# Kernel optimization log

Measured on AMD Instinct MI355X. Metric: run time of the kernel, lower is better.

Reference implementation:

```python
import jax, jax.numpy as jnp
import numpy as np

RC = 5.0
P = 6
N_ATOM = 4
N_AXIS = 8
EPS = 1e-5
C_RES = 0.89442719  # sqrt(0.8)
C_NEW = 0.4472      # ~sqrt(0.2)
BESSEL_PREF = float(np.sqrt(2.0 / RC))


def poly_cutoff(x):
    # nequip-style PolynomialCutoff, p=6
    xr = x / RC
    p = float(P)
    out = (1.0
           - (p + 1.0) * (p + 2.0) / 2.0 * xr ** P
           + p * (p + 2.0) * xr ** (P + 1)
           - p * (p + 1.0) / 2.0 * xr ** (P + 2))
    return jnp.where(xr < 1.0, out, 0.0)


def bessel(x, w):
    # x: [E], w: [n_basis] (trainable n*pi weights)
    return BESSEL_PREF * jnp.sin(w * x[:, None] / RC) / x[:, None]


def layer_norm(x, g, b):
    m = jnp.mean(x, axis=-1, keepdims=True)
    v = jnp.var(x, axis=-1, keepdims=True)
    return (x - m) * jax.lax.rsqrt(v + EPS) * g + b


def mlp3(x, W1, b1, W2, b2, W3, b3):
    # FFN: hidden block (linear-tanh-linear) + tanh + final linear
    h = jnp.tanh(x @ W1 + b1)
    h = jnp.tanh(h @ W2 + b2)
    return h @ W3 + b3


def resnet3(x, W1, b1, W2, b2, W3, b3):
    # ResNet: residual added where in/out dims match (final 64->64 linear)
    h = jnp.tanh(x @ W1 + b1)
    h = h @ W2 + b2
    return jnp.tanh(h) @ W3 + b3 + h


def seg_mean(x, idx, n):
    s = jax.ops.segment_sum(x, idx, num_segments=n)
    c = jax.ops.segment_sum(jnp.ones((x.shape[0],), x.dtype), idx, num_segments=n)
    c = jnp.maximum(c, 1.0).reshape((n,) + (1,) * (x.ndim - 1))
    return s / c


def setup_inputs() -> dict:
    key = jax.random.key(0)
    ks = iter(jax.random.split(key, 64))
    N, E, E2 = 40000, 320000, 160000
    NB, NR, NS, NA = 16, 64, 16, 8
    D = NA * NS  # 128 = n_hidden
    L = 2
    f32 = jnp.float32

    def nrm(shape, s=0.05):
        return jax.random.normal(next(ks), shape, dtype=f32) * s

    inp = {}
    inp['atom_types'] = jax.random.randint(next(ks), (N,), 0, N_ATOM, dtype=jnp.int32)
    ev = jax.random.normal(next(ks), (E, 3), dtype=f32)
    inp['env_vectors'] = ev
    inp['env_length'] = jnp.linalg.norm(ev, axis=-1) + 0.1
    inp['edge_length'] = jax.random.uniform(next(ks), (E2,), dtype=f32) * 4.0 + 0.5
    inp['env_index'] = jax.random.randint(next(ks), (2, E), 0, N, dtype=jnp.int32)
    inp['edge_index'] = jax.random.randint(next(ks), (2, E2), 0, N, dtype=jnp.int32)
    inp['bessel_w'] = jnp.arange(1, NB + 1, dtype=f32) * jnp.pi
    A = 2 * N_ATOM + NB  # 24
    inp['sr_W1'], inp['sr_b1'] = nrm((A, 64)), nrm((64,))
    inp['sr_W2'], inp['sr_b2'] = nrm((64, 64)), nrm((64,))
    inp['sr_W3'], inp['sr_b3'] = nrm((64, NS)), nrm((NS,))
    inp['rd_W1'], inp['rd_b1'] = nrm((A, 64)), nrm((64,))
    inp['rd_W2'], inp['rd_b2'] = nrm((64, 64)), nrm((64,))
    inp['rd_W3'], inp['rd_b3'] = nrm((64, NR)), nrm((NR,))
    inp['ne_emb_W'], inp['ne_emb_b'] = nrm((NR, D)), nrm((D,))
    inp['ne_nln_g'], inp['ne_nln_b'] = jnp.ones((D,), f32), jnp.zeros((D,), f32)
    inp['ne_eln_g'], inp['ne_eln_b'] = jnp.ones((NR,), f32), jnp.zeros((NR,), f32)
    inp['ly_emb_W'], inp['ly_emb_b'] = nrm((L, NR, D)), nrm((L, D))
    inp['ly_hid_W1'], inp['ly_hid_b1'] = nrm((L, 2 * D, 128)), nrm((L, 128))
    inp['ly_hid_W2'], inp['ly_hid_b2'] = nrm((L, 128, 128)), nrm((L, 128))
    inp['ly_hid_W3'], inp['ly_hid_b3'] = nrm((L, 128, D)), nrm((L, D))
    inp['ly_rdl_W1'], inp['ly_rdl_b1'] = nrm((L, NR + D, 64)), nrm((L, 64))
    inp['ly_rdl_W2'], inp['ly_rdl_b2'] = nrm((L, 64, 64)), nrm((L, 64))
    inp['ly_rdl_W3'], inp['ly_rdl_b3'] = nrm((L, 64, NR)), nrm((L, NR))
    inp['ly_nln_g'], inp['ly_nln_b'] = jnp.ones((L, D), f32), jnp.zeros((L, D), f32)
    inp['ly_eln_g'], inp['ly_eln_b'] = jnp.ones((L, NR), f32), jnp.zeros((L, NR), f32)
    return inp


def reference(atom_types, env_vectors, env_length, edge_length, env_index, edge_index,
              bessel_w,
              sr_W1, sr_b1, sr_W2, sr_b2, sr_W3, sr_b3,
              rd_W1, rd_b1, rd_W2, rd_b2, rd_W3, rd_b3,
              ne_emb_W, ne_emb_b, ne_nln_g, ne_nln_b, ne_eln_g, ne_eln_b,
              ly_emb_W, ly_emb_b,
              ly_hid_W1, ly_hid_b1, ly_hid_W2, ly_hid_b2, ly_hid_W3, ly_hid_b3,
              ly_rdl_W1, ly_rdl_b1, ly_rdl_W2, ly_rdl_b2, ly_rdl_W3, ly_rdl_b3,
              ly_nln_g, ly_nln_b, ly_eln_g, ly_eln_b):
    N = atom_types.shape[0]
    oh = jax.nn.one_hot(atom_types, N_ATOM, dtype=env_vectors.dtype)
    # atom_attr[index].transpose(1,0).reshape(E,-1) == concat of the two endpoints' one-hots
    env_attr = jnp.concatenate([oh[env_index[0]], oh[env_index[1]]], -1)   # [E, 2*n_atom]
    edge_attr = jnp.concatenate([oh[edge_index[0]], oh[edge_index[1]]], -1)
    ud_env = poly_cutoff(env_length)[:, None]    # [E, 1]
    ud_edge = poly_cutoff(edge_length)[:, None]  # [E2, 1]
    feat_env = jnp.concatenate([env_attr, ud_env * bessel(env_length, bessel_w)], -1)
    feat_edge = jnp.concatenate([edge_attr, ud_edge * bessel(edge_length, bessel_w)], -1)
    env_sqrt = mlp3(feat_env, sr_W1, sr_b1, sr_W2, sr_b2, sr_W3, sr_b3) * ud_env  # [E, n_sqrt]
    env_radial = layer_norm(mlp3(feat_env, rd_W1, rd_b1, rd_W2, rd_b2, rd_W3, rd_b3), ne_eln_g, ne_eln_b) * ud_env
    edge_radial = layer_norm(mlp3(feat_edge, rd_W1, rd_b1, rd_W2, rd_b2, rd_W3, rd_b3), ne_eln_g, ne_eln_b) * ud_edge
    # SE(2) aggregation: msg = [env_sqrt | ud * env_vectors]; outer product per node
    msg = env_sqrt[:, :, None] * (ud_env * env_vectors)[:, None, :]  # [E, n_sqrt, 3]
    agg = seg_mean(msg, env_index[1], N)                             # [N, n_sqrt, 3]
    gram = jnp.einsum('nds,nes->nde', agg, agg)[:, :, :N_AXIS]       # [N, n_sqrt, n_axis]
    node_emb = layer_norm(gram.reshape(N, -1), ne_nln_g, ne_nln_b)   # [N, D]
    env_hidden = (env_radial @ ne_emb_W + ne_emb_b) * (node_emb[env_index[1]] + node_emb[env_index[0]]) * 0.5
    edge_hidden = (edge_radial @ ne_emb_W + ne_emb_b) * (node_emb[edge_index[1]] + node_emb[edge_index[0]]) * 0.5
    for l in range(ly_emb_W.shape[0]):
        env_weight = env_radial @ ly_emb_W[l] + ly_emb_b[l]  # [E, D]
        agg2 = seg_mean(env_weight * node_emb[env_index[1]], env_index[1], N)
        node_emb = C_RES * node_emb + C_NEW * layer_norm(agg2, ly_nln_g[l], ly_nln_b[l])
        env_hidden = mlp3(jnp.concatenate([node_emb[env_index[0]], env_hidden], -1),
                          ly_hid_W1[l], ly_hid_b1[l], ly_hid_W2[l], ly_hid_b2[l], ly_hid_W3[l], ly_hid_b3[l])
        edge_hidden = mlp3(jnp.concatenate([node_emb[edge_index[0]], edge_hidden], -1),
                           ly_hid_W1[l], ly_hid_b1[l], ly_hid_W2[l], ly_hid_b2[l], ly_hid_W3[l], ly_hid_b3[l])
        env_radial = C_RES * env_radial + C_NEW * ud_env * layer_norm(
            resnet3(jnp.concatenate([env_radial, env_hidden], -1),
                    ly_rdl_W1[l], ly_rdl_b1[l], ly_rdl_W2[l], ly_rdl_b2[l], ly_rdl_W3[l], ly_rdl_b3[l]),
            ly_eln_g[l], ly_eln_b[l])
        edge_radial = C_RES * edge_radial + C_NEW * ud_edge * layer_norm(
            resnet3(jnp.concatenate([edge_radial, edge_hidden], -1),
                    ly_rdl_W1[l], ly_rdl_b1[l], ly_rdl_W2[l], ly_rdl_b2[l], ly_rdl_W3[l], ly_rdl_b3[l]),
            ly_eln_g[l], ly_eln_b[l])
    return env_radial, edge_radial, node_emb, env_hidden, edge_hidden
```

## Files before the change

kernel.cpp:

```cpp
#include <hip/hip_runtime.h>
#include <math.h>

#define C_RES 0.89442719f
#define C_NEW 0.4472f
#define LN_EPS 1e-5f
#define BESSEL_PREF 0.6324555320336759f
#define RC_INV 0.2f

typedef __attribute__((ext_vector_type(8))) short short8;
typedef __attribute__((ext_vector_type(8))) unsigned short u16x8;
typedef __attribute__((ext_vector_type(16))) float f32x16;

__device__ __forceinline__ float fast_tanh(float x) {
  float ax = fabsf(x);
  float e = __expf(2.0f * ax);
  float t = 1.0f - 2.0f / (e + 1.0f);
  return copysignf(t, x);
}

__device__ __forceinline__ unsigned short f2b(float f) {
  unsigned int u = __float_as_uint(f);
  unsigned int r = (u + 0x7FFFu + ((u >> 16) & 1u)) >> 16;
  return (unsigned short)r;
}

__device__ __forceinline__ u16x8 cvt8(const float* s) {
  const float4 v0 = *(const float4*)s;
  const float4 v1 = *(const float4*)(s + 4);
  u16x8 w;
  w[0]=f2b(v0.x); w[1]=f2b(v0.y); w[2]=f2b(v0.z); w[3]=f2b(v0.w);
  w[4]=f2b(v1.x); w[5]=f2b(v1.y); w[6]=f2b(v1.z); w[7]=f2b(v1.w);
  return w;
}

__device__ __forceinline__ short8 cvt8s(const float* s) {
  const float4 v0 = *(const float4*)s;
  const float4 v1 = *(const float4*)(s + 4);
  short8 w;
  w[0]=(short)f2b(v0.x); w[1]=(short)f2b(v0.y); w[2]=(short)f2b(v0.z); w[3]=(short)f2b(v0.w);
  w[4]=(short)f2b(v1.x); w[5]=(short)f2b(v1.y); w[6]=(short)f2b(v1.z); w[7]=(short)f2b(v1.w);
  return w;
}

__device__ __forceinline__ float poly_cutoff(float x) {
  float xr = x * RC_INV;
  if (xr >= 1.0f) return 0.0f;
  float x2 = xr * xr;
  float x3 = x2 * xr;
  float x6 = x3 * x3;
  return 1.0f - 28.0f * x6 + 48.0f * x6 * xr - 21.0f * x6 * x2;
}

__device__ __forceinline__ int swz(int s, int kc) {
  return s ^ ((s >> 5) << 1) ^ ((kc & 1) << 2);
}

// ... 28 lines not shown
      if (lane >= o) incl += t;
    }
    if (lane == 63) wsum[wid] = incl;
    __syncthreads();
    if (wid == 0) {
      const int wv = (lane < 16) ? wsum[lane] : 0;
      int wsc = wv;
      #pragma unroll
      for (int o = 1; o < 16; o <<= 1) {
        const int t = __shfl_up(wsc, o);
        if (lane >= o) wsc += t;
      }
      if (lane < 16) wsum[lane] = wsc - wv;
    }
    __syncthreads();
    const int c0 = carry;
    const int excl = c0 + wsum[wid] + incl - v;
    if (i < n) { eoff[i] = excl; ecur[i] = excl; }
    __syncthreads();
    if (tid == 1023) carry = c0 + wsum[15] + incl;
    __syncthreads();
  }
  if (tid == 0) eoff[n] = carry;
}

__global__ void scatter_kernel(int E, const int* __restrict__ idx,
                               int* __restrict__ ecur, int* __restrict__ perm) {
  int t = blockIdx.x * 256 + threadIdx.x;
  if (t < E) {
    const int pos = atomicAdd(&ecur[idx[E + t]], 1);
    perm[pos] = t;
  }
}

__global__ void pack_hid_weights(const float* __restrict__ W1,
                                 const float* __restrict__ W2,
                                 const float* __restrict__ W3,
                                 unsigned short* __restrict__ out)
{
  int t = blockIdx.x * 256 + threadIdx.x;
  if (t >= 131072) return;
  int l = t >> 16;
  int oidx = t & 65535;
  const float* src;
  int midx;
  if (oidx < 32768)      { src = W1 + l * 32768; midx = oidx; }
  else if (oidx < 49152) { src = W2 + l * 16384; midx = oidx - 32768; }
  else                   { src = W3 + l * 16384; midx = oidx - 49152; }
  int j = midx & 7;
  int lane = (midx >> 3) & 63;
  int blk = midx >> 9;
  int ct = blk & 3, kc = blk >> 2;
  int col = ct * 32 + (lane & 31);
  int k = kc * 16 + (lane >> 5) * 8 + j;
  out[l * 65536 + oidx] = f2b(src[k * 128 + col]);
}

__global__ void pack_rdl_weights(const float* __restrict__ W1,
                                 const float* __restrict__ W2,
                                 const float* __restrict__ W3,
                                 unsigned short* __restrict__ out)
{
  int t = blockIdx.x * 256 + threadIdx.x;
  if (t >= 40960) return;
  int l = t / 20480;
  int o = t - l * 20480;
// ... 37 lines not shown
}

__global__ void pack_emb_weights(const float* __restrict__ W,
                                 unsigned short* __restrict__ out)
{
  int t = blockIdx.x * 256 + threadIdx.x;
  if (t >= 8192) return;
  const int j = t & 7, lane = (t >> 3) & 63, blk = t >> 9;
  const int ct = blk & 3, kc = blk >> 2;
  const int col = ct * 32 + (lane & 31);
  const int k = kc * 16 + (lane >> 5) * 8 + j;
  out[t] = f2b(W[k * 128 + col]);
}


#define FEAT_TRANS(BASEBLK, V0, V1) do {                                        \
    _Pragma("unroll")                                                           \
    for (int ct_ = 0; ct_ < 2; ++ct_) {                                         \
      const int colh_ = ct_*32 + cl;                                            \
      const int kc2_  = colh_ >> 4;                                             \
      const int b3_   = (colh_ >> 3) & 1;                                       \
      const int jj_   = colh_ & 7;                                              \
      const int blk_  = ((BASEBLK) + kc2_*3 + wave)*512;                        \
      _Pragma("unroll")                                                         \
      for (int q_ = 0; q_ < 16; ++q_) {                                         \
        const int row32_ = (q_ & 3) + 8*(q_ >> 2) + 4*(lane >> 5);              \
        const int s2_ = (row32_ & 31) + 32*b3_;                                 \
        const float v_ = ct_ ? (V1)[q_] : (V0)[q_];                             \
        afrag[blk_ + swz(s2_, kc2_)*8 + jj_] = f2b(fast_tanh(v_));              \
      }                                                                         \
    }                                                                           \
  } while (0)

template<int HAS_SR>
__launch_bounds__(192)
__global__ void feat_mfma(
    int nrows,
    const int* __restrict__ types, const float* __restrict__ lens,
    const float* __restrict__ vecs, const int* __restrict__ idx,
    const float* __restrict__ bessel_w,
    const unsigned short* __restrict__ wpackf,
    const float* __restrict__ srb1, const float* __restrict__ srb2,
    const float* __restrict__ srb3,
    const float* __restrict__ rdb1, const float* __restrict__ rdb2,
    const float* __restrict__ rdb3,
    const float* __restrict__ eln_g, const float* __restrict__ eln_b,
    float* __restrict__ radial_out, float* __restrict__ ud_out,
    float* __restrict__ msgbuf)
{
  __shared__ __align__(16) unsigned short afrag[30*512];
  __shared__ __align__(16) unsigned short wlds[36*512];
  __shared__ float udl[96];

  const int tid  = threadIdx.x;
  const int lane = tid & 63;
  const int wave = tid >> 6;
  const int base = blockIdx.x * 96;
  const int cl   = lane & 31;

  for (int i = tid; i < 2304; i += 192)
    *(u16x8*)&wlds[i*8] = *(const u16x8*)&wpackf[i*8];

  {
    const int r = tid >> 1, h = tid & 1;
    int rowc = base + r;
    const bool valid = rowc < nrows;
    if (!valid) rowc = nrows - 1;
    const int i0 = idx[rowc];
    const int i1 = idx[nrows + rowc];
    const float len = lens[rowc];
    const float ud = poly_cutoff(len);
    const int t0 = types[i0], t1 = types[i1];
    const float invl = 1.0f / len;
    const int rt = r >> 5;
    #pragma unroll
    for (int m = 0; m < 12; ++m) {
      const int k = h + m*2;
      float v;
      if (k < 4)      v = (t0 == k) ? 1.0f : 0.0f;
      else if (k < 8) v = (t1 == (k-4)) ? 1.0f : 0.0f;
      else            v = ud * BESSEL_PREF * __sinf(bessel_w[k-8] * len * RC_INV) * invl;
      const int kc = k >> 4;
      const int s_ = (r & 31) + 32*((k >> 3) & 1);
      afrag[(kc*3 + rt)*512 + swz(s_, kc)*8 + (k & 7)] = f2b(v);
    }
    #pragma unroll
    for (int m = 0; m < 4; ++m) {
      const int k = 24 + h + m*2;
      const int s_ = (r & 31) + 32*((k >> 3) & 1);
      afrag[(1*3 + rt)*512 + swz(s_, 1)*8 + (k & 7)] = 0;
    }
    if (h == 0) {
      udl[r] = ud;
      if (valid) {
        ud_out[rowc] = ud;
        if (HAS_SR) {
          msgbuf[(size_t)rowc*20 + 16] = ud * vecs[(size_t)rowc*3 + 0];
          msgbuf[(size_t)rowc*20 + 17] = ud * vecs[(size_t)rowc*3 + 1];
          msgbuf[(size_t)rowc*20 + 18] = ud * vecs[(size_t)rowc*3 + 2];
        }
      }
    }
  }
  __syncthreads();

  f32x16 acc0, acc1;

  {
    const float bv0 = rdb1[cl], bv1 = rdb1[32 + cl];
    #pragma unroll
    for (int q = 0; q < 16; ++q) { acc0[q] = bv0; acc1[q] = bv1; }
  }
  #pragma unroll
  for (int kc = 0; kc < 2; ++kc) {
    const short8 a  = *(const short8*)&afrag[(kc*3 + wave)*512 + swz(lane, kc)*8];
    const short8 w0 = *(const short8*)&wlds[(kc*2 + 0)*512 + lane*8];
    const short8 w1 = *(const short8*)&wlds[(kc*2 + 1)*512 + lane*8];
    acc0 = __builtin_amdgcn_mfma_f32_32x32x16_bf16(a, w0, acc0, 0, 0, 0);
    acc1 = __builtin_amdgcn_mfma_f32_32x32x16_bf16(a, w1, acc1, 0, 0, 0);
  }
  FEAT_TRANS(6, acc0, acc1);

  {
    const float bv0 = rdb2[cl], bv1 = rdb2[32 + cl];
    #pragma unroll
    for (int q = 0; q < 16; ++q) { acc0[q] = bv0; acc1[q] = bv1; }
  }
  #pragma unroll
  for (int kc = 0; kc < 4; ++kc) {
// ... 13 lines not shown
  #pragma unroll
  for (int kc = 0; kc < 4; ++kc) {
    const short8 a  = *(const short8*)&afrag[((18 + kc*3) + wave)*512 + swz(lane, kc)*8];
    const short8 w0 = *(const short8*)&wlds[(12 + kc*2 + 0)*512 + lane*8];
    const short8 w1 = *(const short8*)&wlds[(12 + kc*2 + 1)*512 + lane*8];
    acc0 = __builtin_amdgcn_mfma_f32_32x32x16_bf16(a, w0, acc0, 0, 0, 0);
    acc1 = __builtin_amdgcn_mfma_f32_32x32x16_bf16(a, w1, acc1, 0, 0, 0);
  }
  {
    const float eg0 = eln_g[cl],      eb0 = eln_b[cl];
    const float eg1 = eln_g[32 + cl], eb1 = eln_b[32 + cl];
    #pragma unroll
    for (int q = 0; q < 16; ++q) {
      const float v0 = acc0[q], v1 = acc1[q];
      float s = v0 + v1, ss = v0*v0 + v1*v1;
      #pragma unroll
      for (int o = 1; o <= 16; o <<= 1) {
        s  += __shfl_xor(s, o);
        ss += __shfl_xor(ss, o);
      }
      const float m   = s * (1.0f/64.0f);
      const float inv = rsqrtf(ss * (1.0f/64.0f) - m*m + LN_EPS);
      const int row32 = (q & 3) + 8*(q >> 2) + 4*(lane >> 5);
      const int rloc  = wave*32 + row32;
      const int row   = base + rloc;
      if (row < nrows) {
        const float u = udl[rloc];
        radial_out[(size_t)row*64 + cl]      = ((v0 - m)*inv*eg0 + eb0) * u;
        radial_out[(size_t)row*64 + 32 + cl] = ((v1 - m)*inv*eg1 + eb1) * u;
      }
    }
  }

  if (HAS_SR) {
    {
      const float bv0 = srb1[cl], bv1 = srb1[32 + cl];
      #pragma unroll
      for (int q = 0; q < 16; ++q) { acc0[q] = bv0; acc1[q] = bv1; }
    }
    #pragma unroll
    for (int kc = 0; kc < 2; ++kc) {
      const short8 a  = *(const short8*)&afrag[(kc*3 + wave)*512 + swz(lane, kc)*8];
      const short8 w0 = *(const short8*)&wlds[(20 + kc*2 + 0)*512 + lane*8];
      const short8 w1 = *(const short8*)&wlds[(20 + kc*2 + 1)*512 + lane*8];
      acc0 = __builtin_amdgcn_mfma_f32_32x32x16_bf16(a, w0, acc0, 0, 0, 0);
      acc1 = __builtin_amdgcn_mfma_f32_32x32x16_bf16(a, w1, acc1, 0, 0, 0);
    }
    FEAT_TRANS(6, acc0, acc1);

    {
      const float bv0 = srb2[cl], bv1 = srb2[32 + cl];
      #pragma unroll
      for (int q = 0; q < 16; ++q) { acc0[q] = bv0; acc1[q] = bv1; }
    }
    #pragma unroll
    for (int kc = 0; kc < 4; ++kc) {
      const short8 a  = *(const short8*)&afrag[((6 + kc*3) + wave)*512 + swz(lane, kc)*8];
      const short8 w0 = *(const short8*)&wlds[(24 + kc*2 + 0)*512 + lane*8];
      const short8 w1 = *(const short8*)&wlds[(24 + kc*2 + 1)*512 + lane*8];
      acc0 = __builtin_amdgcn_mfma_f32_32x32x16_bf16(a, w0, acc0, 0, 0, 0);
      acc1 = __builtin_amdgcn_mfma_f32_32x32x16_bf16(a, w1, acc1, 0, 0, 0);
    }
    FEAT_TRANS(18, acc0, acc1);

    {
      const float bv0 = (cl < 16) ? srb3[cl] : 0.0f;
      #pragma unroll
// ... 134 lines not shown
  const float g0 = g[j0], g1 = g[j0+1], g2 = g[j0+2], g3 = g[j0+3];
  const float bb0 = b[j0], bb1 = b[j0+1], bb2 = b[j0+2], bb3 = b[j0+3];
  #pragma unroll
  for (int i = 0; i < 4; ++i) {
    const int n = base + r0 + i;
    if (n >= N) continue;
    const float mask = (ecnt[n] > 0) ? 1.0f : 0.0f;
    const float4 old = *(const float4*)&node_emb[(size_t)n*128 + j0];
    const float x0 = old.x * acc[i][0] * mask;
    const float x1 = old.y * acc[i][1] * mask;
    const float x2 = old.z * acc[i][2] * mask;
    const float x3 = old.w * acc[i][3] * mask;
    float s = x0 + x1 + x2 + x3;
    float ss = x0*x0 + x1*x1 + x2*x2 + x3*x3;
    #pragma unroll
    for (int o = 1; o <= 16; o <<= 1) {
      s  += __shfl_xor(s, o);
      ss += __shfl_xor(ss, o);
    }
    const float m = s * (1.0f/128.0f);
    const float inv = rsqrtf(ss * (1.0f/128.0f) - m*m + LN_EPS);
    float4 o4;
    o4.x = C_RES*old.x + C_NEW*((x0 - m)*inv*g0 + bb0);
    o4.y = C_RES*old.y + C_NEW*((x1 - m)*inv*g1 + bb1);
    o4.z = C_RES*old.z + C_NEW*((x2 - m)*inv*g2 + bb2);
    o4.w = C_RES*old.w + C_NEW*((x3 - m)*inv*g3 + bb3);
    *(float4*)&node_emb[(size_t)n*128 + j0] = o4;
  }
}


__launch_bounds__(192)
__global__ void emb_mfma(
    int nrows,
    const float* __restrict__ radial,
    const unsigned short* __restrict__ wpck, const float* __restrict__ bias,
    const int* __restrict__ idx,
    const float* __restrict__ node_emb,
    float* __restrict__ out)
{
  __shared__ __align__(16) unsigned short afrag[12*512];
  __shared__ __align__(16) unsigned short wlds[16*512];
  __shared__ int i0l[96], i1l[96];

  const int tid = threadIdx.x, lane = tid & 63, wave = tid >> 6;
  const int base = blockIdx.x * 96, cl = lane & 31;

  for (int i = tid; i < 1024; i += 192)
    *(u16x8*)&wlds[i*8] = *(const u16x8*)&wpck[i*8];

  {
    const int r = tid >> 1, h = tid & 1;
    int rowg = base + r;
    if (rowg >= nrows) rowg = nrows - 1;
    if (h == 0) { i0l[r] = idx[rowg]; i1l[r] = idx[nrows + rowg]; }
    const float* rsrc = radial + (size_t)rowg * 64;
    #pragma unroll
    for (int g = 0; g < 4; ++g) {
      const int k = h*32 + g*8;
      const u16x8 w = cvt8(rsrc + k);
      const int kc = k >> 4;
      const int s_ = (r & 31) + 32*((k >> 3) & 1);
      *(u16x8*)&afrag[(kc*3 + (r>>5))*512 + swz(s_, kc)*8] = w;
    }
  }
  __syncthreads();

  f32x16 acc0, acc1, acc2, acc3;
  {
    const float bv0 = bias[cl], bv1 = bias[32+cl];
    const float bv2 = bias[64+cl], bv3 = bias[96+cl];
    #pragma unroll
    for (int q = 0; q < 16; ++q) { acc0[q]=bv0; acc1[q]=bv1; acc2[q]=bv2; acc3[q]=bv3; }
  }
  #pragma unroll
  for (int kc = 0; kc < 4; ++kc) {
    const short8 a  = *(const short8*)&afrag[(kc*3 + wave)*512 + swz(lane, kc)*8];
    const short8 w0 = *(const short8*)&wlds[(kc*4 + 0)*512 + lane*8];
    const short8 w1 = *(const short8*)&wlds[(kc*4 + 1)*512 + lane*8];
// ... 2 lines not shown
    acc0 = __builtin_amdgcn_mfma_f32_32x32x16_bf16(a, w0, acc0, 0, 0, 0);
    acc1 = __builtin_amdgcn_mfma_f32_32x32x16_bf16(a, w1, acc1, 0, 0, 0);
    acc2 = __builtin_amdgcn_mfma_f32_32x32x16_bf16(a, w2, acc2, 0, 0, 0);
    acc3 = __builtin_amdgcn_mfma_f32_32x32x16_bf16(a, w3, acc3, 0, 0, 0);
  }

  #pragma unroll
  for (int q = 0; q < 16; ++q) {
    const int row32 = (q & 3) + 8*(q >> 2) + 4*(lane >> 5);
    const int rloc  = wave*32 + row32;
    const int row   = base + rloc;
    if (row >= nrows) continue;
    const float* n0 = node_emb + (size_t)i0l[rloc]*128;
    const float* n1 = node_emb + (size_t)i1l[rloc]*128;
    float* op = out + (size_t)row*128;
    op[cl]    = acc0[q] * 0.5f * (n0[cl]    + n1[cl]);
    op[32+cl] = acc1[q] * 0.5f * (n0[32+cl] + n1[32+cl]);
    op[64+cl] = acc2[q] * 0.5f * (n0[64+cl] + n1[64+cl]);
    op[96+cl] = acc3[q] * 0.5f * (n0[96+cl] + n1[96+cl]);
  }
}


#define STAGE_WG(SRC, OFFU16, B) do {                                           \
    _Pragma("unroll")                                                           \
    for (int i_ = 0; i_ < 2; ++i_) {                                            \
      const int c_ = tid + i_*256;                                              \
      *(u16x8*)&wg[B][c_*8] = *(const u16x8*)&(SRC)[(OFFU16) + c_*8];           \
    }                                                                           \
  } while (0)

__launch_bounds__(256, 3)
__global__ void hidrdl_mfma(
    int nrows, const int* __restrict__ idx0,
    const float* __restrict__ node_emb,
    const float* __restrict__ ud,
    const unsigned short* __restrict__ wpackh,
    const float* __restrict__ hb1, const float* __restrict__ hb2,
    const float* __restrict__ hb3,
    const unsigned short* __restrict__ wpackr,
    const float* __restrict__ rb1, const float* __restrict__ rb2,
    const float* __restrict__ rb3,
    const float* __restrict__ eln_g, const float* __restrict__ eln_b,
    float* __restrict__ hidden,
    float* __restrict__ radial)
{
  __shared__ __align__(16) unsigned short afragH[16384];
  __shared__ __align__(16) unsigned short wg[2][4096];

  const int tid  = threadIdx.x;
  const int lane = tid & 63;
  const int wave = tid >> 6;
  const int base = blockIdx.x * 128;
  const int cl   = lane & 31;
  const int khalf = lane >> 5;

  int lrow = base + wave*32 + cl;
  if (lrow >= nrows) lrow = nrows - 1;
  const int i0 = idx0[lrow];
  const float* nsrc = node_emb + (size_t)i0 * 128;
  const float* hsrc = hidden + (size_t)lrow * 128;
  const float* rsrc = radial + (size_t)lrow * 64;

  short8 aN[8], aH[8];
  #pragma unroll
  for (int kc = 0; kc < 8; ++kc) aN[kc] = cvt8s(nsrc + kc*16 + khalf*8);
  #pragma unroll
  for (int kc = 0; kc < 8; ++kc) aH[kc] = cvt8s(hsrc + kc*16 + khalf*8);

  f32x16 acc[4];

  #pragma unroll
  for (int ct = 0; ct < 4; ++ct) {
    const float bv = hb1[ct*32 + cl];
    #pragma unroll
    for (int q = 0; q < 16; ++q) acc[ct][q] = bv;
  }
  STAGE_WG(wpackh, 0, 0);
  __syncthreads();
  #pragma unroll
  for (int p = 0; p < 8; ++p) {
    if (p < 7) STAGE_WG(wpackh, (p+1)*4096, (p+1)&1);
    else       STAGE_WG(wpackh, 32768, 0);
    #pragma unroll
    for (int kcl = 0; kcl < 2; ++kcl) {
      const int kc = p*2 + kcl;
      const short8 a = (kc < 8) ? aN[kc] : aH[kc-8];
      #pragma unroll
      for (int ct = 0; ct < 4; ++ct) {
        const short8 b = *(const short8*)&wg[p&1][ (kcl*4 + ct)*512 + lane*8 ];
        acc[ct] = __builtin_amdgcn_mfma_f32_32x32x16_bf16(a, b, acc[ct], 0, 0, 0);
      }
    }
    __syncthreads();
  }

  #pragma unroll
  for (int ct = 0; ct < 4; ++ct) {
    const int kc  = ct*2 + ((lane >> 4) & 1);
    const int oct = (lane >> 3) & 1;
    const int j   = lane & 7;
    const int xk  = (oct << 1) ^ ((kc & 1) << 2);
    const int hi  = 4*(lane >> 5);
    const int bi  = (wave*8 + kc)*512 + oct*256 + j;
    #pragma unroll
    for (int q = 0; q < 16; ++q) {
      const int m32 = (q & 3) + 8*(q >> 2) + hi;
      afragH[bi + (m32 ^ xk)*8] = f2b(fast_tanh(acc[ct][q]));
    }
  }

  #pragma unroll
  for (int ct = 0; ct < 4; ++ct) {
    const float bv = hb2[ct*32 + cl];
    #pragma unroll
    for (int q = 0; q < 16; ++q) acc[ct][q] = bv;
  }
  #pragma unroll
  for (int p = 0; p < 4; ++p) {
    if (p < 3) STAGE_WG(wpackh, 32768 + (p+1)*4096, (p+1)&1);
    else       STAGE_WG(wpackh, 49152, 0);
    #pragma unroll
    for (int kcl = 0; kcl < 2; ++kcl) {
      const int kc = p*2 + kcl;
      const short8 a = *(const short8*)&afragH[ (wave*8 + kc)*512 + swz(lane, kc)*8 ];
      #pragma unroll
      for (int ct = 0; ct < 4; ++ct) {
        const short8 b = *(const short8*)&wg[p&1][ (kcl*4 + ct)*512 + lane*8 ];
        acc[ct] = __builtin_amdgcn_mfma_f32_32x32x16_bf16(a, b, acc[ct], 0, 0, 0);
      }
    }
    __syncthreads();
  }

  #pragma unroll
  for (int ct = 0; ct < 4; ++ct) {
    const int kc  = ct*2 + ((lane >> 4) & 1);
    const int oct = (lane >> 3) & 1;
    const int j   = lane & 7;
    const int xk  = (oct << 1) ^ ((kc & 1) << 2);
    const int hi  = 4*(lane >> 5);
    const int bi  = (wave*8 + kc)*512 + oct*256 + j;
    #pragma unroll
    for (int q = 0; q < 16; ++q) {
      const int m32 = (q & 3) + 8*(q >> 2) + hi;
      afragH[bi + (m32 ^ xk)*8] = f2b(fast_tanh(acc[ct][q]));
    }
  }

  #pragma unroll
  for (int ct = 0; ct < 4; ++ct) {
    const float bv = hb3[ct*32 + cl];
    #pragma unroll
    for (int q = 0; q < 16; ++q) acc[ct][q] = bv;
  }
  #pragma unroll
  for (int p = 0; p < 4; ++p) {
    if (p < 3) STAGE_WG(wpackh, 49152 + (p+1)*4096, (p+1)&1);
    else       STAGE_WG(wpackr, 0, 0);
    #pragma unroll
    for (int kcl = 0; kcl < 2; ++kcl) {
      const int kc = p*2 + kcl;
      const short8 a = *(const short8*)&afragH[ (wave*8 + kc)*512 + swz(lane, kc)*8 ];
      #pragma unroll
      for (int ct = 0; ct < 4; ++ct) {
        const short8 b = *(const short8*)&wg[p&1][ (kcl*4 + ct)*512 + lane*8 ];
        acc[ct] = __builtin_amdgcn_mfma_f32_32x32x16_bf16(a, b, acc[ct], 0, 0, 0);
      }
    }
    __syncthreads();
  }

  #pragma unroll
  for (int ct = 0; ct < 4; ++ct) {
    const int col = ct*32 + cl;
    #pragma unroll
    for (int q = 0; q < 16; ++q) {
      const int row = base + wave*32 + (q & 3) + 8*(q >> 2) + 4*khalf;
      if (row < nrows) hidden[(size_t)row*128 + col] = acc[ct][q];
    }
  }
  #pragma unroll
  for (int ct = 0; ct < 4; ++ct) {
    const int kc  = ct*2 + ((lane >> 4) & 1);
    const int oct = (lane >> 3) & 1;
    const int j   = lane & 7;
    const int xk  = (oct << 1) ^ ((kc & 1) << 2);
    const int hi  = 4*(lane >> 5);
    const int bi  = (wave*8 + kc)*512 + oct*256 + j;
    #pragma unroll
    for (int q = 0; q < 16; ++q) {
      const int m32 = (q & 3) + 8*(q >> 2) + hi;
      afragH[bi + (m32 ^ xk)*8] = f2b(acc[ct][q]);
    }
  }

  short8 aR[4];
  #pragma unroll
  for (int kc = 0; kc < 4; ++kc) aR[kc] = cvt8s(rsrc + kc*16 + khalf*8);

  f32x16 racc0, racc1;
  {
    const float bv0 = rb1[cl], bv1 = rb1[32 + cl];
    #pragma unroll
    for (int q = 0; q < 16; ++q) { racc0[q] = bv0; racc1[q] = bv1; }
  }
  #pragma unroll
  for (int t = 0; t < 3; ++t) {
    if (t < 2) STAGE_WG(wpackr, (t+1)*4096, (t+1)&1);
    else       STAGE_WG(wpackr, 12288, 1);
    #pragma unroll
    for (int kk = 0; kk < 4; ++kk) {
      const int kc = t*4 + kk;
      const short8 a = (kc < 4) ? aR[kc]
        : *(const short8*)&afragH[ (wave*8 + (kc-4))*512 + swz(lane, kc-4)*8 ];
      const short8 w0 = *(const short8*)&wg[t&1][ (kk*2 + 0)*512 + lane*8 ];
      const short8 w1 = *(const short8*)&wg[t&1][ (kk*2 + 1)*512 + lane*8 ];
      racc0 = __builtin_amdgcn_mfma_f32_32x32x16_bf16(a, w0, racc0, 0, 0, 0);
      racc1 = __builtin_amdgcn_mfma_f32_32x32x16_bf16(a, w1, racc1, 0, 0, 0);
    }
    __syncthreads();
  }

  #pragma unroll
  for (int ct = 0; ct < 2; ++ct) {
    const int colh = ct*32 + cl;
    const int kc2  = colh >> 4;
    const int b3_  = (colh >> 3) & 1;
    const int jj   = colh & 7;
    const int blk  = (wave*8 + kc2)*512;
    #pragma unroll
    for (int q = 0; q < 16; ++q) {
      const int row32 = (q & 3) + 8*(q >> 2) + 4*khalf;
      const int s_ = (row32 & 31) + 32*b3_;
      const float v = ct ? racc1[q] : racc0[q];
      afragH[blk + swz(s_, kc2)*8 + jj] = f2b(fast_tanh(v));
    }
  }

  f32x16 rh0, rh1;
  {
    const float bv0 = rb2[cl], bv1 = rb2[32 + cl];
    #pragma unroll
    for (int q = 0; q < 16; ++q) { rh0[q] = bv0; rh1[q] = bv1; }
  }
  STAGE_WG(wpackr, 16384, 0);
  #pragma unroll
  for (int kc = 0; kc < 4; ++kc) {
    const short8 a  = *(const short8*)&afragH[ (wave*8 + kc)*512 + swz(lane, kc)*8 ];
    const short8 w0 = *(const short8*)&wg[1][ (kc*2 + 0)*512 + lane*8 ];
    const short8 w1 = *(const short8*)&wg[1][ (kc*2 + 1)*512 + lane*8 ];
    rh0 = __builtin_amdgcn_mfma_f32_32x32x16_bf16(a, w0, rh0, 0, 0, 0);
    rh1 = __builtin_amdgcn_mfma_f32_32x32x16_bf16(a, w1, rh1, 0, 0, 0);
  }
  __syncthreads();

  #pragma unroll
  for (int ct = 0; ct < 2; ++ct) {
    const int colh = ct*32 + cl;
    const int kc2  = colh >> 4;
    const int b3_  = (colh >> 3) & 1;
    const int jj   = colh & 7;
    const int blk  = (wave*8 + 4 + kc2)*512;
    #pragma unroll
    for (int q = 0; q < 16; ++q) {
      const int row32 = (q & 3) + 8*(q >> 2) + 4*khalf;
      const int s_ = (row32 & 31) + 32*b3_;
      const float v = ct ? rh1[q] : rh0[q];
      afragH[blk + swz(s_, kc2)*8 + jj] = f2b(fast_tanh(v));
    }
  }

  {
    const float bv0 = rb3[cl], bv1 = rb3[32 + cl];
    #pragma unroll
    for (int q = 0; q < 16; ++q) { racc0[q] = bv0; racc1[q] = bv1; }
  }
  #pragma unroll
  for (int kc = 0; kc < 4; ++kc) {
    const short8 a  = *(const short8*)&afragH[ (wave*8 + 4 + kc)*512 + swz(lane, kc)*8 ];
    const short8 w0 = *(const short8*)&wg[0][ (kc*2 + 0)*512 + lane*8 ];
    const short8 w1 = *(const short8*)&wg[0][ (kc*2 + 1)*512 + lane*8 ];
    racc0 = __builtin_amdgcn_mfma_f32_32x32x16_bf16(a, w0, racc0, 0, 0, 0);
    racc1 = __builtin_amdgcn_mfma_f32_32x32x16_bf16(a, w1, racc1, 0, 0, 0);
  }

  const float eg0 = eln_g[cl],      eb0 = eln_b[cl];
  const float eg1 = eln_g[32 + cl], eb1 = eln_b[32 + cl];
  const float* rtile = radial + (size_t)(base + wave*32) * 64;

  #pragma unroll
  for (int q = 0; q < 16; ++q) {
    const float v0 = racc0[q] + rh0[q];
    const float v1 = racc1[q] + rh1[q];
    float s = v0 + v1, ss = v0*v0 + v1*v1;
    #pragma unroll
    for (int o = 1; o <= 16; o <<= 1) {
      s  += __shfl_xor(s, o);
      ss += __shfl_xor(ss, o);
    }
    const float m   = s * (1.0f/64.0f);
    const float inv = rsqrtf(ss * (1.0f/64.0f) - m*m + LN_EPS);
    const int row32 = (q & 3) + 8*(q >> 2) + 4*khalf;
    const int row   = base + wave*32 + row32;
    if (row < nrows) {
      const float u = ud[row];
      const float oldA = rtile[row32*64 + cl];
      const float oldB = rtile[row32*64 + 32 + cl];
      radial[(size_t)row*64 + cl]      = C_RES*oldA + C_NEW*u*((v0 - m)*inv*eg0 + eb0);
      radial[(size_t)row*64 + 32 + cl] = C_RES*oldB + C_NEW*u*((v1 - m)*inv*eg1 + eb1);
    }
  }
}


extern "C" void kernel_launch(void* const* d_in, const int* in_sizes, int n_in,
                              void* d_out, int out_size, void* d_ws, size_t ws_size,
                              hipStream_t stream)
{
  const int*   atom_types = (const int*)  d_in[0];
  const float* env_vec    = (const float*)d_in[1];
  const float* env_len    = (const float*)d_in[2];
  const float* edge_len   = (const float*)d_in[3];
  const int*   env_idx    = (const int*)  d_in[4];
  const int*   edge_idx   = (const int*)  d_in[5];
  const float* bessel_w   = (const float*)d_in[6];
  const float* srW1 = (const float*)d_in[7];  const float* srb1 = (const float*)d_in[8];
  const float* srW2 = (const float*)d_in[9];  const float* srb2 = (const float*)d_in[10];
  const float* srW3 = (const float*)d_in[11]; const float* srb3 = (const float*)d_in[12];
  const float* rdW1 = (const float*)d_in[13]; const float* rdb1 = (const float*)d_in[14];
  const float* rdW2 = (const float*)d_in[15]; const float* rdb2 = (const float*)d_in[16];
  const float* rdW3 = (const float*)d_in[17]; const float* rdb3 = (const float*)d_in[18];
  const float* ne_emb_W = (const float*)d_in[19]; const float* ne_emb_b = (const float*)d_in[20];
  const float* ne_nln_g = (const float*)d_in[21]; const float* ne_nln_b = (const float*)d_in[22];
  const float* ne_eln_g = (const float*)d_in[23]; const float* ne_eln_b = (const float*)d_in[24];
  const float* ly_emb_W = (const float*)d_in[25]; const float* ly_emb_b = (const float*)d_in[26];
  const float* ly_hid_W1 = (const float*)d_in[27]; const float* ly_hid_b1 = (const float*)d_in[28];
  const float* ly_hid_W2 = (const float*)d_in[29]; const float* ly_hid_b2 = (const float*)d_in[30];
  const float* ly_hid_W3 = (const float*)d_in[31]; const float* ly_hid_b3 = (const float*)d_in[32];
  const float* ly_rdl_W1 = (const float*)d_in[33]; const float* ly_rdl_b1 = (const float*)d_in[34];
  const float* ly_rdl_W2 = (const float*)d_in[35]; const float* ly_rdl_b2 = (const float*)d_in[36];
  const float* ly_rdl_W3 = (const float*)d_in[37]; const float* ly_rdl_b3 = (const float*)d_in[38];
  const float* ly_nln_g = (const float*)d_in[39]; const float* ly_nln_b = (const float*)d_in[40];
// ... 12 lines not shown

  float* ws = (float*)d_ws;
  float* ud_env  = ws;  ws += E;
  float* ud_edge = ws;  ws += E2;
  float* aggS    = ws;  ws += (size_t)N * 48;
  float* msgbuf  = ws;  ws += (size_t)E * 20;
  float* mean_r  = msgbuf;
  unsigned short* wpack  = (unsigned short*)ws; ws += 65536;
  unsigned short* wpack2 = (unsigned short*)ws; ws += 20480;
  unsigned short* wpack3 = (unsigned short*)ws; ws += 9216;
  unsigned short* wpackE = (unsigned short*)ws; ws += 4096;
  int* ecnt = (int*)ws; ws += N;
  int* eoff = (int*)ws; ws += N + 1;
  int* ecur = (int*)ws; ws += N + 1;
  int* perm = (int*)ws; ws += E;

  const int gEr  = (E  + 95) / 96;
  const int gE2r = (E2 + 95) / 96;
  const int gEf  = (E  + 127) / 128;
  const int gE2f = (E2 + 127) / 128;
  const int gN32 = (N + 31) / 32;
  const int gN4w = (N * 64 + 255) / 256;

  zero_int_kernel<<<256, 256, 0, stream>>>(ecnt, N);
  hist_kernel<<<(E + 255) / 256, 256, 0, stream>>>(E, env_idx, ecnt);
  scan_kernel<<<1, 1024, 0, stream>>>(ecnt, eoff, ecur, N);
  scatter_kernel<<<(E + 255) / 256, 256, 0, stream>>>(E, env_idx, ecur, perm);

  pack_hid_weights<<<512, 256, 0, stream>>>(ly_hid_W1, ly_hid_W2, ly_hid_W3, wpack);
  pack_rdl_weights<<<160, 256, 0, stream>>>(ly_rdl_W1, ly_rdl_W2, ly_rdl_W3, wpack2);
  pack_feat_weights<<<72, 256, 0, stream>>>(rdW1, rdW2, rdW3, srW1, srW2, srW3, wpack3);
  pack_emb_weights<<<32, 256, 0, stream>>>(ne_emb_W, wpackE);

  feat_mfma<1><<<gEr, 192, 0, stream>>>(E, atom_types, env_len, env_vec, env_idx, bessel_w,
      wpack3, srb1, srb2, srb3, rdb1, rdb2, rdb3,
      ne_eln_g, ne_eln_b, env_radial, ud_env, msgbuf);
  feat_mfma<0><<<gE2r, 192, 0, stream>>>(E2, atom_types, edge_len, nullptr, edge_idx, bessel_w,
      wpack3, srb1, srb2, srb3, rdb1, rdb2, rdb3,
      ne_eln_g, ne_eln_b, edge_radial, ud_edge, nullptr);

  msg_gather_kernel<<<gN4w, 256, 0, stream>>>(N, eoff, perm, msgbuf, aggS);
  node_emb_kernel<<<N, 128, 0, stream>>>(N, aggS, ecnt, ne_nln_g, ne_nln_b, node_emb);

  emb_mfma<<<gEr, 192, 0, stream>>>(E, env_radial, wpackE, ne_emb_b, env_idx, node_emb, env_hidden);
  emb_mfma<<<gE2r, 192, 0, stream>>>(E2, edge_radial, wpackE, ne_emb_b, edge_idx, node_emb, edge_hidden);

  for (int l = 0; l < 2; ++l) {
    agg_gather_kernel<<<gN4w, 256, 0, stream>>>(N, eoff, perm, env_radial, mean_r);
    node_update_gemm<<<gN32, 256, 0, stream>>>(N, mean_r, ecnt,
        ly_emb_W + (size_t)l*64*128, ly_emb_b + (size_t)l*128,
        ly_nln_g + (size_t)l*128, ly_nln_b + (size_t)l*128, node_emb);

    hidrdl_mfma<<<gEf, 256, 0, stream>>>(E, env_idx, node_emb, ud_env,
        wpack + (size_t)l*65536,
        ly_hid_b1 + (size_t)l*128, ly_hid_b2 + (size_t)l*128, ly_hid_b3 + (size_t)l*128,
        wpack2 + (size_t)l*20480,
        ly_rdl_b1 + (size_t)l*64, ly_rdl_b2 + (size_t)l*64, ly_rdl_b3 + (size_t)l*64,
        ly_eln_g + (size_t)l*64, ly_eln_b + (size_t)l*64,
        env_hidden, env_radial);
    hidrdl_mfma<<<gE2f, 256, 0, stream>>>(E2, edge_idx, node_emb, ud_edge,
        wpack + (size_t)l*65536,
        ly_hid_b1 + (size_t)l*128, ly_hid_b2 + (size_t)l*128, ly_hid_b3 + (size_t)l*128,
        wpack2 + (size_t)l*20480,
        ly_rdl_b1 + (size_t)l*64, ly_rdl_b2 + (size_t)l*64, ly_rdl_b3 + (size_t)l*64,
        ly_eln_g + (size_t)l*64, ly_eln_b + (size_t)l*64,
        edge_hidden, edge_radial);
  }
}
```

Before: 1.312 ms.

## Merge env/edge launches and stage hidrdl outputs through LDS for coalesced stores

Fuses the paired env and edge launches of feat_mfma, emb_mfma and hidrdl_mfma into single grids. Each block selects its pointer set by block index, which removes launch gaps and tail underutilisation. In hidrdl_mfma, the hidden and radial outputs are staged in LDS as bf16 and then written with row-contiguous float4 stores instead of strided scalar stores. This truncates the stored fp32 outputs to bf16 precision, which may cause accuracy drift.

```diff
diff --git a/kernel.cpp b/kernel.cpp
--- a/kernel.cpp
+++ b/kernel.cpp
@@ -22,6 +22,10 @@
   unsigned int u = __float_as_uint(f);
   unsigned int r = (u + 0x7FFFu + ((u >> 16) & 1u)) >> 16;
   return (unsigned short)r;
+}
+
+__device__ __forceinline__ float b2f(unsigned short v) {
+  return __uint_as_float((unsigned)v << 16);
 }
 
 __device__ __forceinline__ u16x8 cvt8(const float* s) {
@@ -116,6 +120,7 @@
     perm[pos] = t;
   }
 }
+
 
 __global__ void pack_hid_weights(const float* __restrict__ W1,
                                  const float* __restrict__ W2,
@@ -219,12 +224,13 @@
     }                                                                           \
   } while (0)
 
-template<int HAS_SR>
 __launch_bounds__(192)
 __global__ void feat_mfma(
-    int nrows,
-    const int* __restrict__ types, const float* __restrict__ lens,
-    const float* __restrict__ vecs, const int* __restrict__ idx,
+    int g1, int n1, const float* __restrict__ lens1, const int* __restrict__ idx1,
+    float* __restrict__ radial1, float* __restrict__ ud1,
+    int n2, const float* __restrict__ lens2, const int* __restrict__ idx2,
+    float* __restrict__ radial2, float* __restrict__ ud2,
+    const int* __restrict__ types, const float* __restrict__ vecs,
     const float* __restrict__ bessel_w,
     const unsigned short* __restrict__ wpackf,
     const float* __restrict__ srb1, const float* __restrict__ srb2,
@@ -232,7 +238,6 @@
     const float* __restrict__ rdb1, const float* __restrict__ rdb2,
     const float* __restrict__ rdb3,
     const float* __restrict__ eln_g, const float* __restrict__ eln_b,
-    float* __restrict__ radial_out, float* __restrict__ ud_out,
     float* __restrict__ msgbuf)
 {
   __shared__ __align__(16) unsigned short afrag[30*512];
@@ -242,8 +247,14 @@
   const int tid  = threadIdx.x;
   const int lane = tid & 63;
   const int wave = tid >> 6;
-  const int base = blockIdx.x * 96;
   const int cl   = lane & 31;
+
+  int blk = blockIdx.x;
+  const bool has_sr = (blk < g1);
+  int nrows; const float* lens; const int* idx; float* radial_out; float* ud_out;
+  if (has_sr) { nrows = n1; lens = lens1; idx = idx1; radial_out = radial1; ud_out = ud1; }
+  else { blk -= g1; nrows = n2; lens = lens2; idx = idx2; radial_out = radial2; ud_out = ud2; }
+  const int base = blk * 96;
 
   for (int i = tid; i < 2304; i += 192)
     *(u16x8*)&wlds[i*8] = *(const u16x8*)&wpackf[i*8];
@@ -281,7 +292,7 @@
       udl[r] = ud;
       if (valid) {
         ud_out[rowc] = ud;
-        if (HAS_SR) {
+        if (has_sr) {
           msgbuf[(size_t)rowc*20 + 16] = ud * vecs[(size_t)rowc*3 + 0];
           msgbuf[(size_t)rowc*20 + 17] = ud * vecs[(size_t)rowc*3 + 1];
           msgbuf[(size_t)rowc*20 + 18] = ud * vecs[(size_t)rowc*3 + 2];
@@ -361,7 +372,7 @@
     }
   }
 
-  if (HAS_SR) {
+  if (has_sr) {
     {
       const float bv0 = srb1[cl], bv1 = srb1[32 + cl];
       #pragma unroll
@@ -562,19 +573,25 @@
 
 __launch_bounds__(192)
 __global__ void emb_mfma(
-    int nrows,
-    const float* __restrict__ radial,
+    int g1, int n1, const float* __restrict__ radial1, const int* __restrict__ idx1,
+    float* __restrict__ out1,
+    int n2, const float* __restrict__ radial2, const int* __restrict__ idx2,
+    float* __restrict__ out2,
     const unsigned short* __restrict__ wpck, const float* __restrict__ bias,
-    const int* __restrict__ idx,
-    const float* __restrict__ node_emb,
-    float* __restrict__ out)
+    const float* __restrict__ node_emb)
 {
   __shared__ __align__(16) unsigned short afrag[12*512];
   __shared__ __align__(16) unsigned short wlds[16*512];
   __shared__ int i0l[96], i1l[96];
 
   const int tid = threadIdx.x, lane = tid & 63, wave = tid >> 6;
-  const int base = blockIdx.x * 96, cl = lane & 31;
+  const int cl = lane & 31;
+
+  int blk = blockIdx.x;
+  int nrows; const float* radial; const int* idx; float* out;
+  if (blk < g1) { nrows = n1; radial = radial1; idx = idx1; out = out1; }
+  else { blk -= g1; nrows = n2; radial = radial2; idx = idx2; out = out2; }
+  const int base = blk * 96;
 
   for (int i = tid; i < 1024; i += 192)
     *(u16x8*)&wlds[i*8] = *(const u16x8*)&wpck[i*8];
@@ -643,18 +660,19 @@
 
 __launch_bounds__(256, 3)
 __global__ void hidrdl_mfma(
-    int nrows, const int* __restrict__ idx0,
+    int g1,
+    int n1, const int* __restrict__ idx1, const float* __restrict__ ud1,
+    float* __restrict__ hid1, float* __restrict__ rad1,
+    int n2, const int* __restrict__ idx2, const float* __restrict__ ud2,
+    float* __restrict__ hid2, float* __restrict__ rad2,
     const float* __restrict__ node_emb,
-    const float* __restrict__ ud,
     const unsigned short* __restrict__ wpackh,
     const float* __restrict__ hb1, const float* __restrict__ hb2,
     const float* __restrict__ hb3,
     const unsigned short* __restrict__ wpackr,
     const float* __restrict__ rb1, const float* __restrict__ rb2,
     const float* __restrict__ rb3,
-    const float* __restrict__ eln_g, const float* __restrict__ eln_b,
-    float* __restrict__ hidden,
-    float* __restrict__ radial)
+    const float* __restrict__ eln_g, const float* __restrict__ eln_b)
 {
   __shared__ __align__(16) unsigned short afragH[16384];
   __shared__ __align__(16) unsigned short wg[2][4096];
@@ -662,9 +680,14 @@
   const int tid  = threadIdx.x;
   const int lane = tid & 63;
   const int wave = tid >> 6;
-  const int base = blockIdx.x * 128;
   const int cl   = lane & 31;
   const int khalf = lane >> 5;
+
+  int blk = blockIdx.x;
+  int nrows; const int* idx0; const float* ud; float* hidden; float* radial;
+  if (blk < g1) { nrows = n1; idx0 = idx1; ud = ud1; hidden = hid1; radial = rad1; }
+  else { blk -= g1; nrows = n2; idx0 = idx2; ud = ud2; hidden = hid2; radial = rad2; }
+  const int base = blk * 128;
 
   int lrow = base + wave*32 + cl;
   if (lrow >= nrows) lrow = nrows - 1;
@@ -712,7 +735,7 @@
     const int oct = (lane >> 3) & 1;
     const int j   = lane & 7;
     const int xk  = (oct << 1) ^ ((kc & 1) << 2);
-    const int hi  = 4*(lane >> 5);
+    const int hi  = 4*khalf;
     const int bi  = (wave*8 + kc)*512 + oct*256 + j;
     #pragma unroll
     for (int q = 0; q < 16; ++q) {
@@ -750,7 +773,7 @@
     const int oct = (lane >> 3) & 1;
     const int j   = lane & 7;
     const int xk  = (oct << 1) ^ ((kc & 1) << 2);
-    const int hi  = 4*(lane >> 5);
+    const int hi  = 4*khalf;
     const int bi  = (wave*8 + kc)*512 + oct*256 + j;
     #pragma unroll
     for (int q = 0; q < 16; ++q) {
@@ -784,25 +807,39 @@
 
   #pragma unroll
   for (int ct = 0; ct < 4; ++ct) {
-    const int col = ct*32 + cl;
-    #pragma unroll
-    for (int q = 0; q < 16; ++q) {
-      const int row = base + wave*32 + (q & 3) + 8*(q >> 2) + 4*khalf;
-      if (row < nrows) hidden[(size_t)row*128 + col] = acc[ct][q];
-    }
-  }
-  #pragma unroll
-  for (int ct = 0; ct < 4; ++ct) {
     const int kc  = ct*2 + ((lane >> 4) & 1);
     const int oct = (lane >> 3) & 1;
     const int j   = lane & 7;
     const int xk  = (oct << 1) ^ ((kc & 1) << 2);
-    const int hi  = 4*(lane >> 5);
+    const int hi  = 4*khalf;
     const int bi  = (wave*8 + kc)*512 + oct*256 + j;
     #pragma unroll
     for (int q = 0; q < 16; ++q) {
       const int m32 = (q & 3) + 8*(q >> 2) + hi;
       afragH[bi + (m32 ^ xk)*8] = f2b(acc[ct][q]);
+    }
+  }
+  {
+    const int rloc = tid >> 1;
+    const int hh = tid & 1;
+    const int row = base + rloc;
+    if (row < nrows) {
+      float* hp = hidden + (size_t)row*128 + hh*64;
+      #pragma unroll
+      for (int g = 0; g < 4; ++g) {
+        const int kc = hh*4 + g;
+        const u16x8 lo = *(const u16x8*)&afragH[(wave*8 + kc)*512 + swz((rloc & 31),      kc)*8];
+        const u16x8 hi2 = *(const u16x8*)&afragH[(wave*8 + kc)*512 + swz((rloc & 31) + 32, kc)*8];
+        float4 f0, f1, f2, f3;
+        f0.x = b2f(lo[0]); f0.y = b2f(lo[1]); f0.z = b2f(lo[2]); f0.w = b2f(lo[3]);
+        f1.x = b2f(lo[4]); f1.y = b2f(lo[5]); f1.z = b2f(lo[6]); f1.w = b2f(lo[7]);
+        f2.x = b2f(hi2[0]); f2.y = b2f(hi2[1]); f2.z = b2f(hi2[2]); f2.w = b2f(hi2[3]);
+        f3.x = b2f(hi2[4]); f3.y = b2f(hi2[5]); f3.z = b2f(hi2[6]); f3.w = b2f(hi2[7]);
+        *(float4*)(hp + g*16 + 0)  = f0;
+        *(float4*)(hp + g*16 + 4)  = f1;
+        *(float4*)(hp + g*16 + 8)  = f2;
+        *(float4*)(hp + g*16 + 12) = f3;
+      }
     }
   }
 
@@ -839,13 +876,13 @@
     const int kc2  = colh >> 4;
     const int b3_  = (colh >> 3) & 1;
     const int jj   = colh & 7;
-    const int blk  = (wave*8 + kc2)*512;
+    const int blk2 = (wave*8 + kc2)*512;
     #pragma unroll
     for (int q = 0; q < 16; ++q) {
       const int row32 = (q & 3) + 8*(q >> 2) + 4*khalf;
       const int s_ = (row32 & 31) + 32*b3_;
       const float v = ct ? racc1[q] : racc0[q];
-      afragH[blk + swz(s_, kc2)*8 + jj] = f2b(fast_tanh(v));
+      afragH[blk2 + swz(s_, kc2)*8 + jj] = f2b(fast_tanh(v));
     }
   }
 
@@ -872,13 +909,13 @@
     const int kc2  = colh >> 4;
     const int b3_  = (colh >> 3) & 1;
     const int jj   = colh & 7;
-    const int blk  = (wave*8 + 4 + kc2)*512;
+    const int blk2 = (wave*8 + 4 + kc2)*512;
     #pragma unroll
     for (int q = 0; q < 16; ++q) {
       const int row32 = (q & 3) + 8*(q >> 2) + 4*khalf;
       const int s_ = (row32 & 31) + 32*b3_;
       const float v = ct ? rh1[q] : rh0[q];
-      afragH[blk + swz(s_, kc2)*8 + jj] = f2b(fast_tanh(v));
+      afragH[blk2 + swz(s_, kc2)*8 + jj] = f2b(fast_tanh(v));
     }
   }
 
@@ -899,6 +936,7 @@
   const float eg0 = eln_g[cl],      eb0 = eln_b[cl];
   const float eg1 = eln_g[32 + cl], eb1 = eln_b[32 + cl];
   const float* rtile = radial + (size_t)(base + wave*32) * 64;
+  unsigned short* rstg = &afragH[wave*4*512];
 
   #pragma unroll
   for (int q = 0; q < 16; ++q) {
@@ -914,12 +952,34 @@
     const float inv = rsqrtf(ss * (1.0f/64.0f) - m*m + LN_EPS);
     const int row32 = (q & 3) + 8*(q >> 2) + 4*khalf;
     const int row   = base + wave*32 + row32;
+    const int xr = (row32 & 7) << 3;
     if (row < nrows) {
       const float u = ud[row];
       const float oldA = rtile[row32*64 + cl];
       const float oldB = rtile[row32*64 + 32 + cl];
-      radial[(size_t)row*64 + cl]      = C_RES*oldA + C_NEW*u*((v0 - m)*inv*eg0 + eb0);
-      radial[(size_t)row*64 + 32 + cl] = C_RES*oldB + C_NEW*u*((v1 - m)*inv*eg1 + eb1);
+      rstg[row32*64 + (cl ^ xr)]        = f2b(C_RES*oldA + C_NEW*u*((v0 - m)*inv*eg0 + eb0));
+      rstg[row32*64 + ((32 + cl) ^ xr)] = f2b(C_RES*oldB + C_NEW*u*((v1 - m)*inv*eg1 + eb1));
+    }
+  }
+  {
+    const int rloc = tid >> 1;
+    const int hh = tid & 1;
+    const int row = base + rloc;
+    if (row < nrows) {
+      const int r32 = rloc & 31;
+      const int xr = (r32 & 7);
+      unsigned short* rs = &afragH[(rloc >> 5)*4*512 + r32*64];
+      float* rp = radial + (size_t)row*64 + hh*32;
+      #pragma unroll
+      for (int g = 0; g < 4; ++g) {
+        const int c3 = hh*4 + g;
+        const u16x8 v = *(const u16x8*)&rs[(c3 ^ xr)*8];
+        float4 f0, f1;
+        f0.x = b2f(v[0]); f0.y = b2f(v[1]); f0.z = b2f(v[2]); f0.w = b2f(v[3]);
+        f1.x = b2f(v[4]); f1.y = b2f(v[5]); f1.z = b2f(v[6]); f1.w = b2f(v[7]);
+        *(float4*)(rp + g*8 + 0) = f0;
+        *(float4*)(rp + g*8 + 4) = f1;
+      }
     }
   }
 }
@@ -998,18 +1058,20 @@
   pack_feat_weights<<<72, 256, 0, stream>>>(rdW1, rdW2, rdW3, srW1, srW2, srW3, wpack3);
   pack_emb_weights<<<32, 256, 0, stream>>>(ne_emb_W, wpackE);
 
-  feat_mfma<1><<<gEr, 192, 0, stream>>>(E, atom_types, env_len, env_vec, env_idx, bessel_w,
-      wpack3, srb1, srb2, srb3, rdb1, rdb2, rdb3,
-      ne_eln_g, ne_eln_b, env_radial, ud_env, msgbuf);
-  feat_mfma<0><<<gE2r, 192, 0, stream>>>(E2, atom_types, edge_len, nullptr, edge_idx, bessel_w,
-      wpack3, srb1, srb2, srb3, rdb1, rdb2, rdb3,
-      ne_eln_g, ne_eln_b, edge_radial, ud_edge, nullptr);
+  feat_mfma<<<gEr + gE2r, 192, 0, stream>>>(
+      gEr, E, env_len, env_idx, env_radial, ud_env,
+      E2, edge_len, edge_idx, edge_radial, ud_edge,
+      atom_types, env_vec, bessel_w, wpack3,
+      srb1, srb2, srb3, rdb1, rdb2, rdb3,
+      ne_eln_g, ne_eln_b, msgbuf);
 
   msg_gather_kernel<<<gN4w, 256, 0, stream>>>(N, eoff, perm, msgbuf, aggS);
   node_emb_kernel<<<N, 128, 0, stream>>>(N, aggS, ecnt, ne_nln_g, ne_nln_b, node_emb);
 
-  emb_mfma<<<gEr, 192, 0, stream>>>(E, env_radial, wpackE, ne_emb_b, env_idx, node_emb, env_hidden);
-  emb_mfma<<<gE2r, 192, 0, stream>>>(E2, edge_radial, wpackE, ne_emb_b, edge_idx, node_emb, edge_hidden);
+  emb_mfma<<<gEr + gE2r, 192, 0, stream>>>(
+      gEr, E, env_radial, env_idx, env_hidden,
+      E2, edge_radial, edge_idx, edge_hidden,
+      wpackE, ne_emb_b, node_emb);
 
   for (int l = 0; l < 2; ++l) {
     agg_gather_kernel<<<gN4w, 256, 0, stream>>>(N, eoff, perm, env_radial, mean_r);
@@ -1017,19 +1079,15 @@
         ly_emb_W + (size_t)l*64*128, ly_emb_b + (size_t)l*128,
         ly_nln_g + (size_t)l*128, ly_nln_b + (size_t)l*128, node_emb);
 
-    hidrdl_mfma<<<gEf, 256, 0, stream>>>(E, env_idx, node_emb, ud_env,
+    hidrdl_mfma<<<gEf + gE2f, 256, 0, stream>>>(
+        gEf,
+        E, env_idx, ud_env, env_hidden, env_radial,
+        E2, edge_idx, ud_edge, edge_hidden, edge_radial,
+        node_emb,
         wpack + (size_t)l*65536,
         ly_hid_b1 + (size_t)l*128, ly_hid_b2 + (size_t)l*128, ly_hid_b3 + (size_t)l*128,
         wpack2 + (size_t)l*20480,
         ly_rdl_b1 + (size_t)l*64, ly_rdl_b2 + (size_t)l*64, ly_rdl_b3 + (size_t)l*64,
-        ly_eln_g + (size_t)l*64, ly_eln_b + (size_t)l*64,
-        env_hidden, env_radial);
-    hidrdl_mfma<<<gE2f, 256, 0, stream>>>(E2, edge_idx, node_emb, ud_edge,
-        wpack + (size_t)l*65536,
-        ly_hid_b1 + (size_t)l*128, ly_hid_b2 + (size_t)l*128, ly_hid_b3 + (size_t)l*128,
-        wpack2 + (size_t)l*20480,
-        ly_rdl_b1 + (size_t)l*64, ly_rdl_b2 + (size_t)l*64, ly_rdl_b3 + (size_t)l*64,
-        ly_eln_g + (size_t)l*64, ly_eln_b + (size_t)l*64,
-        edge_hidden, edge_radial);
-  }
-}
+        ly_eln_g + (size_t)l*64, ly_eln_b + (size_t)l*64);
+  }
+}
```

After: 1.350 ms. 1.03x slower.
